# Kernel tuning notes

Measured on AMD Instinct MI355X. Metric: run time of the kernel, lower is better.

## Reference

```python
import jax, jax.numpy as jnp
import numpy as np

B, S, D = 4, 2048, 1024
E, TOPK = 8, 2
SCALE = 0.02


def setup_inputs() -> dict:
    key = jax.random.key(0)
    ks = jax.random.split(key, 7)
    return {
        "x": jax.random.normal(ks[0], (B, S, D), dtype=jnp.float32),
        "router_w": jax.random.normal(ks[1], (D, E), dtype=jnp.float32) * SCALE,
        "router_b": jnp.zeros((E,), dtype=jnp.float32),
        "up_w": jax.random.normal(ks[2], (E, D, 8 * D), dtype=jnp.float32) * SCALE,
        "up_b": jnp.zeros((E, 8 * D), dtype=jnp.float32),
        "down_w": jax.random.normal(ks[3], (E, 4 * D, D), dtype=jnp.float32) * SCALE,
        "down_b": jnp.zeros((E, D), dtype=jnp.float32),
    }


def reference(x, router_w, router_b, up_w, up_b, down_w, down_b):
    b, s, d = x.shape
    flat_x = x.reshape(-1, d)                      # [T, d], T = b*s
    # --- routing ---
    logits = flat_x @ router_w + router_b          # [T, E]
    topk_logits, topk_idx = jax.lax.top_k(logits, TOPK)   # [T, K]
    topk_probs = jax.nn.softmax(topk_logits, axis=-1)     # softmax over the top-k only
    # per-token per-expert combine weight: w[t,e] = sum_k p[t,k] * 1[idx[t,k]==e]
    combine = jnp.sum(
        jax.nn.one_hot(topk_idx, E, dtype=flat_x.dtype) * topk_probs[..., None],
        axis=1,
    )                                              # [T, E]
    # --- experts (dense per-expert compute, masked combine; faithful math) ---
    out = jnp.zeros_like(flat_x)
    for e in range(E):
        h = flat_x @ up_w[e] + up_b[e]             # [T, 8d]
        a, g = jnp.split(h, 2, axis=-1)            # GLU halves, each [T, 4d]
        y = (a * jax.nn.gelu(g, approximate=False)) @ down_w[e] + down_b[e]  # [T, d]
        out = out + combine[:, e:e + 1] * y
    return out.reshape(b, s, d)
```

## Files before the change

### kernel.cpp

```cpp
#include <hip/hip_runtime.h>
#include <hip/hip_bf16.h>

typedef unsigned short u16;
typedef __attribute__((ext_vector_type(8))) short short8;
typedef __attribute__((ext_vector_type(8))) __bf16 bfrag;
typedef __attribute__((ext_vector_type(4))) float cfrag;

#define T_TOK   8192
#define D_MODEL 1024
#define E_EXP   8
#define DFF     4096
#define NPAIR   16384
#define MAXTILE 136

__device__ __forceinline__ u16 f2bf(float f) {
    __hip_bfloat16 h = __float2bfloat16(f);
    return __builtin_bit_cast(u16, h);
}
__device__ __forceinline__ void gld_lds16(const u16* g, u16* l) {
    __builtin_amdgcn_global_load_lds(
        (const __attribute__((address_space(1))) void*)g,
        (__attribute__((address_space(3))) void*)l, 16, 0, 0);
}
__device__ __forceinline__ cfrag mfma16(bfrag a, bfrag b, cfrag c) {
    return __builtin_amdgcn_mfma_f32_16x16x32_bf16(a, b, c, 0, 0, 0);
}

__global__ __launch_bounds__(256) void k_zero(int* cnt) {
    if (threadIdx.x < 64) cnt[threadIdx.x] = 0;
}

__global__ __launch_bounds__(256) void k_route(
    const float* __restrict__ x, const float* __restrict__ rw, const float* __restrict__ rb,
    int* __restrict__ tope, float* __restrict__ wpair, int* __restrict__ cnt)
{
    __shared__ float rws[D_MODEL * E_EXP];
    int tid = threadIdx.x;
    for (int i = tid; i < D_MODEL * E_EXP; i += 256) rws[i] = rw[i];
    __syncthreads();
    int wid = tid >> 6, lane = tid & 63;
    int t = blockIdx.x * 4 + wid;
    const float4* xp = (const float4*)(x + (size_t)t * D_MODEL + lane * 16);
    float xv[16];
#pragma unroll
    for (int j = 0; j < 4; j++) {
        float4 v = xp[j];
        xv[4 * j] = v.x; xv[4 * j + 1] = v.y; xv[4 * j + 2] = v.z; xv[4 * j + 3] = v.w;
    }
    float acc[E_EXP];
#pragma unroll
    for (int e = 0; e < E_EXP; e++) acc[e] = 0.f;
#pragma unroll
    for (int i = 0; i < 16; i++) {
        float xf = xv[i];
        const float* r = &rws[(lane * 16 + i) * E_EXP];
#pragma unroll
        for (int e = 0; e < E_EXP; e++) acc[e] += xf * r[e];
    }
#pragma unroll
    for (int e = 0; e < E_EXP; e++) {
        float v = acc[e];
#pragma unroll
        for (int s = 32; s > 0; s >>= 1) v += __shfl_xor(v, s, 64);
        acc[e] = v;
    }
    if (lane == 0) {
        float lg[E_EXP];
#pragma unroll
        for (int e = 0; e < E_EXP; e++) lg[e] = acc[e] + rb[e];
        int e0 = 0;
        for (int e = 1; e < E_EXP; e++) if (lg[e] > lg[e0]) e0 = e;
        int e1 = -1;
        for (int e = 0; e < E_EXP; e++) {
            if (e == e0) continue;
            if (e1 < 0 || lg[e] > lg[e1]) e1 = e;
        }
        float p0 = 1.f / (1.f + expf(lg[e1] - lg[e0]));
        tope[2 * t] = e0;  tope[2 * t + 1] = e1;
        wpair[2 * t] = p0; wpair[2 * t + 1] = 1.f - p0;
        atomicAdd(&cnt[e0], 1); atomicAdd(&cnt[e1], 1);
    }
}

__global__ void k_scan(const int* __restrict__ cnt, int* __restrict__ cursor,
                       int4* __restrict__ table, int* __restrict__ ntiles)
{
    if (threadIdx.x == 0 && blockIdx.x == 0) {
        int off[E_EXP + 1]; off[0] = 0;
        for (int e = 0; e < E_EXP; e++) off[e + 1] = off[e] + cnt[e];
        for (int e = 0; e < E_EXP; e++) cursor[e] = off[e];
        int nt = 0;
        for (int e = 0; e < E_EXP; e++)
            for (int r = off[e]; r < off[e + 1]; r += 128)
                table[nt++] = make_int4(e, r, off[e + 1], 0);
        *ntiles = nt;
    }
}

__global__ __launch_bounds__(256) void k_permute(
    const int* __restrict__ tope, const float* __restrict__ wpair,
    int* __restrict__ cursor, int* __restrict__ perm,
    int* __restrict__ inv, float* __restrict__ wperm)
{
    int i = blockIdx.x * 256 + threadIdx.x;
    int e = tope[i];
    int p = atomicAdd(&cursor[e], 1);
    perm[p] = i; inv[i] = p; wperm[p] = wpair[i];
}

__global__ __launch_bounds__(256) void k_cvt_x(
    const float* __restrict__ x, u16* __restrict__ xb)
{
    int i = blockIdx.x * 256 + threadIdx.x;
    const float4* xp = (const float4*)(x + (size_t)i * 8);
    float4 v0 = xp[0], v1 = xp[1];
    short8 o;
    o[0] = (short)f2bf(v0.x); o[1] = (short)f2bf(v0.y);
    o[2] = (short)f2bf(v0.z); o[3] = (short)f2bf(v0.w);
    o[4] = (short)f2bf(v1.x); o[5] = (short)f2bf(v1.y);
    o[6] = (short)f2bf(v1.z); o[7] = (short)f2bf(v1.w);
    *(short8*)(xb + (size_t)i * 8) = o;
}

__global__ __launch_bounds__(256) void k_transpose(
    const float* __restrict__ W, u16* __restrict__ WT, int K, int N)
{
    __shared__ u16 tile[64][65];
    int e = blockIdx.z;
    const float* Wp = W + (size_t)e * K * N;
    u16* Tp = WT + (size_t)e * K * N;
    int n0 = blockIdx.x * 64, k0 = blockIdx.y * 64;
    int t = threadIdx.x;
    int rr = t >> 4, cc = (t & 15) * 4;
#pragma unroll
    for (int it = 0; it < 4; ++it) {
        int kr = rr + it * 16;
        float4 v = *(const float4*)(Wp + (size_t)(k0 + kr) * N + n0 + cc);
        tile[kr][cc + 0] = f2bf(v.x); tile[kr][cc + 1] = f2bf(v.y);
        tile[kr][cc + 2] = f2bf(v.z); tile[kr][cc + 3] = f2bf(v.w);
    }
    __syncthreads();
    int nr2 = t >> 3, cc2 = (t & 7) * 8;
#pragma unroll
    for (int it = 0; it < 2; ++it) {
        int nr = nr2 + it * 32;
        short8 v;
#pragma unroll
        for (int i = 0; i < 8; i++) v[i] = (short)tile[cc2 + i][nr];
        *(short8*)(Tp + (size_t)(n0 + nr) * K + k0 + cc2) = v;
    }
}

__global__ __launch_bounds__(256, 2) void k_up_glu(
    const u16* __restrict__ xb, const u16* __restrict__ upT, const float* __restrict__ upb,
    const int* __restrict__ perm, const int4* __restrict__ table,
    const int* __restrict__ ntiles, u16* __restrict__ act)
{
    if ((int)blockIdx.x >= *ntiles) return;
    int4 ti = table[blockIdx.x];
    int e = ti.x, row0 = ti.y, rend = ti.z;
    int n0 = blockIdx.y * 64;
    __shared__ __align__(16) u16 As[128 * 32];
    __shared__ __align__(16) u16 Bs[2][64 * 32];
    int tid = threadIdx.x, lane = tid & 63, wid = tid >> 6;
    int ar = tid >> 2, kc = (tid & 3) * 8;
    int t1 = perm[min(row0 + ar,       rend - 1)] >> 1;
    int t2 = perm[min(row0 + ar + 64,  rend - 1)] >> 1;
    const u16* ga1 = xb + (size_t)t1 * D_MODEL + kc;
    const u16* ga2 = xb + (size_t)t2 * D_MODEL + kc;
    const u16* gb0 = upT + ((size_t)e * 2 * DFF + n0 + ar) * D_MODEL + kc;
    const u16* gb1 = gb0 + (size_t)DFF * D_MODEL;
    u16* lA0 = As + wid * 16 * 32;
    u16* lA1 = As + (64 + wid * 16) * 32;
    u16* lB0 = Bs[0] + wid * 16 * 32;
    u16* lB1 = Bs[1] + wid * 16 * 32;
    cfrag acc[2][4][2];
#pragma unroll
    for (int h = 0; h < 2; h++)
#pragma unroll
        for (int m = 0; m < 4; m++)
#pragma unroll
            for (int n = 0; n < 2; n++) acc[h][m][n] = (cfrag)0.f;
    int wrow = (wid >> 1) * 64, wcol = (wid & 1) * 32;
    int qoff = (lane >> 4) * 8;
    for (int k0 = 0; k0 < D_MODEL; k0 += 32) {
        __syncthreads();
        gld_lds16(ga1, lA0); gld_lds16(ga2, lA1);
        gld_lds16(gb0, lB0); gld_lds16(gb1, lB1);
        ga1 += 32; ga2 += 32; gb0 += 32; gb1 += 32;
        __syncthreads();
        bfrag af[4];
#pragma unroll
        for (int m = 0; m < 4; m++)
            af[m] = __builtin_bit_cast(bfrag, *(const short8*)&As[(wrow + m * 16 + (lane & 15)) * 32 + qoff]);
#pragma unroll
        for (int h = 0; h < 2; h++) {
#pragma unroll
            for (int n = 0; n < 2; n++) {
                bfrag bv = __builtin_bit_cast(bfrag, *(const short8*)&Bs[h][(wcol + n * 16 + (lane & 15)) * 32 + qoff]);
#pragma unroll
                for (int m = 0; m < 4; m++) acc[h][m][n] = mfma16(af[m], bv, acc[h][m][n]);
            }
        }
    }
    const float* ub = upb + (size_t)e * 2 * DFF;
#pragma unroll
    for (int m = 0; m < 4; m++) {
        int rbase = row0 + wrow + m * 16 + ((lane >> 4) << 2);
#pragma unroll
        for (int n = 0; n < 2; n++) {
            int j = n0 + wcol + n * 16 + (lane & 15);
            float ba = ub[j];
            float bg = ub[j + DFF];
#pragma unroll
            for (int r = 0; r < 4; r++) {
                int p = rbase + r;
                if (p < rend) {
                    float a = acc[0][m][n][r] + ba;
                    float g = acc[1][m][n][r] + bg;
                    float gl = 0.5f * g * (1.f + erff(g * 0.70710678118f));
                    act[(size_t)p * DFF + j] = f2bf(a * gl);
                }
            }
        }
    }
}

__global__ __launch_bounds__(256, 2) void k_down(
    const u16* __restrict__ act, const u16* __restrict__ dT, const float* __restrict__ db,
    const float* __restrict__ wperm, const int4* __restrict__ table,
    const int* __restrict__ ntiles, float* __restrict__ ys)
{
    if ((int)blockIdx.x >= *ntiles) return;
    int4 ti = table[blockIdx.x];
    int e = ti.x, row0 = ti.y, rend = ti.z;
    int n0 = blockIdx.y * 128;
    __shared__ __align__(16) u16 As[128 * 32];
    __shared__ __align__(16) u16 Bs[128 * 32];
    int tid = threadIdx.x, lane = tid & 63, wid = tid >> 6;
    int ar = tid >> 2, kc = (tid & 3) * 8;
    int p1 = min(row0 + ar,      rend - 1);
    int p2 = min(row0 + ar + 64, rend - 1);
    const u16* ga1 = act + (size_t)p1 * DFF + kc;
    const u16* ga2 = act + (size_t)p2 * DFF + kc;
    const u16* gb1 = dT + ((size_t)e * D_MODEL + n0 + ar) * DFF + kc;
    const u16* gb2 = gb1 + (size_t)64 * DFF;
    u16* lA0 = As + wid * 16 * 32;
    u16* lA1 = As + (64 + wid * 16) * 32;
    u16* lB0 = Bs + wid * 16 * 32;
    u16* lB1 = Bs + (64 + wid * 16) * 32;
    cfrag acc[4][4];
#pragma unroll
    for (int m = 0; m < 4; m++)
#pragma unroll
        for (int n = 0; n < 4; n++) acc[m][n] = (cfrag)0.f;
    int wrow = (wid >> 1) * 64, wcol = (wid & 1) * 64;
    int qoff = (lane >> 4) * 8;
    for (int k0 = 0; k0 < DFF; k0 += 32) {
        __syncthreads();
        gld_lds16(ga1, lA0); gld_lds16(ga2, lA1);
        gld_lds16(gb1, lB0); gld_lds16(gb2, lB1);
        ga1 += 32; ga2 += 32; gb1 += 32; gb2 += 32;
        __syncthreads();
        bfrag af[4], bv[4];
#pragma unroll
        for (int m = 0; m < 4; m++)
            af[m] = __builtin_bit_cast(bfrag, *(const short8*)&As[(wrow + m * 16 + (lane & 15)) * 32 + qoff]);
#pragma unroll
        for (int n = 0; n < 4; n++)
            bv[n] = __builtin_bit_cast(bfrag, *(const short8*)&Bs[(wcol + n * 16 + (lane & 15)) * 32 + qoff]);
#pragma unroll
        for (int m = 0; m < 4; m++)
#pragma unroll
            for (int n = 0; n < 4; n++) acc[m][n] = mfma16(af[m], bv[n], acc[m][n]);
    }
    const float* dbp = db + (size_t)e * D_MODEL;
#pragma unroll
    for (int m = 0; m < 4; m++) {
        int rbase = row0 + wrow + m * 16 + ((lane >> 4) << 2);
#pragma unroll
        for (int n = 0; n < 4; n++) {
            int col = n0 + wcol + n * 16 + (lane & 15);
            float bias = dbp[col];
#pragma unroll
            for (int r = 0; r < 4; r++) {
                int p = rbase + r;
                if (p < rend)
                    ys[(size_t)p * D_MODEL + col] = (acc[m][n][r] + bias) * wperm[p];
            }
        }
    }
}

__global__ __launch_bounds__(256) void k_combine(
    const float* __restrict__ ys, const int* __restrict__ inv, float* __restrict__ out)
{
    int i = blockIdx.x * 256 + threadIdx.x;
    int t = i >> 8;
    int c = (i & 255) << 2;
    int r0 = inv[2 * t], r1 = inv[2 * t + 1];
    float4 a = *(const float4*)&ys[(size_t)r0 * D_MODEL + c];
    float4 b = *(const float4*)&ys[(size_t)r1 * D_MODEL + c];
    float4 o = make_float4(a.x + b.x, a.y + b.y, a.z + b.z, a.w + b.w);
    *(float4*)&out[(size_t)t * D_MODEL + c] = o;
}

extern "C" void kernel_launch(void* const* d_in, const int* in_sizes, int n_in,
                              void* d_out, int out_size, void* d_ws, size_t ws_size,
                              hipStream_t stream)
{
    const float* x   = (const float*)d_in[0];
    const float* rw  = (const float*)d_in[1];
    const float* rb  = (const float*)d_in[2];
    const float* upw = (const float*)d_in[3];
    const float* upb = (const float*)d_in[4];
    const float* dw  = (const float*)d_in[5];
    const float* db  = (const float*)d_in[6];
    float* out = (float*)d_out;

    char* ws = (char*)d_ws;
    size_t o = 0;
    auto alloc = [&](size_t bytes) -> char* {
        char* p = ws + o; o += (bytes + 255) & ~(size_t)255; return p;
    };
    u16*  upT = (u16*)alloc((size_t)E_EXP * 2 * DFF * D_MODEL * 2);
    u16*  dT  = (u16*)alloc((size_t)E_EXP * D_MODEL * DFF * 2);
    u16*  xb  = (u16*)alloc((size_t)T_TOK * D_MODEL * 2);
    u16*  act = (u16*)alloc((size_t)NPAIR * DFF * 2);
    float* ysb = (float*)upT;
    int*   tope  = (int*)alloc(NPAIR * 4);
    float* wpair = (float*)alloc(NPAIR * 4);
    int*   perm  = (int*)alloc(NPAIR * 4);
    int*   inv   = (int*)alloc(NPAIR * 4);
    float* wperm = (float*)alloc(NPAIR * 4);
    int*   cnt    = (int*)alloc(64 * 4);
    int*   cursor = (int*)alloc(64 * 4);
    int4*  table  = (int4*)alloc(160 * 16);
    int*   ntiles = (int*)alloc(256);
    (void)in_sizes; (void)n_in; (void)out_size; (void)ws_size;

    k_zero<<<1, 256, 0, stream>>>(cnt);
    k_route<<<T_TOK / 4, 256, 0, stream>>>(x, rw, rb, tope, wpair, cnt);
    k_scan<<<1, 64, 0, stream>>>(cnt, cursor, table, ntiles);
    k_permute<<<NPAIR / 256, 256, 0, stream>>>(tope, wpair, cursor, perm, inv, wperm);
    k_cvt_x<<<(T_TOK * D_MODEL / 8) / 256, 256, 0, stream>>>(x, xb);
    k_transpose<<<dim3(8192 / 64, 1024 / 64, E_EXP), 256, 0, stream>>>(upw, upT, 1024, 8192);
    k_transpose<<<dim3(1024 / 64, 4096 / 64, E_EXP), 256, 0, stream>>>(dw, dT, 4096, 1024);
    k_up_glu<<<dim3(MAXTILE, DFF / 64), 256, 0, stream>>>(xb, upT, upb, perm, table, ntiles, act);
    k_down<<<dim3(MAXTILE, D_MODEL / 128), 256, 0, stream>>>(act, dT, db, wperm, table, ntiles, ysb);
    k_combine<<<(T_TOK * D_MODEL / 4) / 256, 256, 0, stream>>>(ysb, inv, out);
}
```

Baseline: 1.481 ms.

## Fuse x bf16 conversion into router and widen GEMM N-tiles

```diff
diff --git a/kernel.cpp b/kernel.cpp
--- a/kernel.cpp
+++ b/kernel.cpp
@@ -32,7 +32,8 @@
 
 __global__ __launch_bounds__(256) void k_route(
     const float* __restrict__ x, const float* __restrict__ rw, const float* __restrict__ rb,
-    int* __restrict__ tope, float* __restrict__ wpair, int* __restrict__ cnt)
+    int* __restrict__ tope, float* __restrict__ wpair, int* __restrict__ cnt,
+    u16* __restrict__ xb)
 {
     __shared__ float rws[D_MODEL * E_EXP];
     int tid = threadIdx.x;
@@ -47,6 +48,13 @@
         float4 v = xp[j];
         xv[4 * j] = v.x; xv[4 * j + 1] = v.y; xv[4 * j + 2] = v.z; xv[4 * j + 3] = v.w;
     }
+    short8 o0, o1;
+#pragma unroll
+    for (int j = 0; j < 8; j++) { o0[j] = (short)f2bf(xv[j]); o1[j] = (short)f2bf(xv[8 + j]); }
+    u16* xbp = xb + (size_t)t * D_MODEL + lane * 16;
+    *(short8*)xbp = o0;
+    *(short8*)(xbp + 8) = o1;
+
     float acc[E_EXP];
 #pragma unroll
     for (int e = 0; e < E_EXP; e++) acc[e] = 0.f;
@@ -108,20 +116,6 @@
     perm[p] = i; inv[i] = p; wperm[p] = wpair[i];
 }
 
-__global__ __launch_bounds__(256) void k_cvt_x(
-    const float* __restrict__ x, u16* __restrict__ xb)
-{
-    int i = blockIdx.x * 256 + threadIdx.x;
-    const float4* xp = (const float4*)(x + (size_t)i * 8);
-    float4 v0 = xp[0], v1 = xp[1];
-    short8 o;
-    o[0] = (short)f2bf(v0.x); o[1] = (short)f2bf(v0.y);
-    o[2] = (short)f2bf(v0.z); o[3] = (short)f2bf(v0.w);
-    o[4] = (short)f2bf(v1.x); o[5] = (short)f2bf(v1.y);
-    o[6] = (short)f2bf(v1.z); o[7] = (short)f2bf(v1.w);
-    *(short8*)(xb + (size_t)i * 8) = o;
-}
-
 __global__ __launch_bounds__(256) void k_transpose(
     const float* __restrict__ W, u16* __restrict__ WT, int K, int N)
 {
@@ -159,35 +153,41 @@
     if ((int)blockIdx.x >= *ntiles) return;
     int4 ti = table[blockIdx.x];
     int e = ti.x, row0 = ti.y, rend = ti.z;
-    int n0 = blockIdx.y * 64;
+    int n0 = blockIdx.y * 128;
     __shared__ __align__(16) u16 As[128 * 32];
-    __shared__ __align__(16) u16 Bs[2][64 * 32];
+    __shared__ __align__(16) u16 Bs[2][128 * 32];
     int tid = threadIdx.x, lane = tid & 63, wid = tid >> 6;
     int ar = tid >> 2, kc = (tid & 3) * 8;
     int t1 = perm[min(row0 + ar,       rend - 1)] >> 1;
     int t2 = perm[min(row0 + ar + 64,  rend - 1)] >> 1;
     const u16* ga1 = xb + (size_t)t1 * D_MODEL + kc;
     const u16* ga2 = xb + (size_t)t2 * D_MODEL + kc;
-    const u16* gb0 = upT + ((size_t)e * 2 * DFF + n0 + ar) * D_MODEL + kc;
-    const u16* gb1 = gb0 + (size_t)DFF * D_MODEL;
-    u16* lA0 = As + wid * 16 * 32;
-    u16* lA1 = As + (64 + wid * 16) * 32;
-    u16* lB0 = Bs[0] + wid * 16 * 32;
-    u16* lB1 = Bs[1] + wid * 16 * 32;
-    cfrag acc[2][4][2];
+    const u16* gb0a = upT + ((size_t)e * 2 * DFF + n0 + ar) * D_MODEL + kc;
+    const u16* gb0b = gb0a + (size_t)64 * D_MODEL;
+    const u16* gb1a = gb0a + (size_t)DFF * D_MODEL;
+    const u16* gb1b = gb1a + (size_t)64 * D_MODEL;
+    u16* lA0  = As + wid * 16 * 32;
+    u16* lA1  = As + (64 + wid * 16) * 32;
+    u16* lB0a = Bs[0] + wid * 16 * 32;
+    u16* lB0b = Bs[0] + (64 + wid * 16) * 32;
+    u16* lB1a = Bs[1] + wid * 16 * 32;
+    u16* lB1b = Bs[1] + (64 + wid * 16) * 32;
+    cfrag acc[2][4][4];
 #pragma unroll
     for (int h = 0; h < 2; h++)
 #pragma unroll
         for (int m = 0; m < 4; m++)
 #pragma unroll
-            for (int n = 0; n < 2; n++) acc[h][m][n] = (cfrag)0.f;
-    int wrow = (wid >> 1) * 64, wcol = (wid & 1) * 32;
+            for (int n = 0; n < 4; n++) acc[h][m][n] = (cfrag)0.f;
+    int wrow = (wid >> 1) * 64, wcol = (wid & 1) * 64;
     int qoff = (lane >> 4) * 8;
     for (int k0 = 0; k0 < D_MODEL; k0 += 32) {
         __syncthreads();
-        gld_lds16(ga1, lA0); gld_lds16(ga2, lA1);
-        gld_lds16(gb0, lB0); gld_lds16(gb1, lB1);
-        ga1 += 32; ga2 += 32; gb0 += 32; gb1 += 32;
+        gld_lds16(ga1, lA0);  gld_lds16(ga2, lA1);
+        gld_lds16(gb0a, lB0a); gld_lds16(gb0b, lB0b);
+        gld_lds16(gb1a, lB1a); gld_lds16(gb1b, lB1b);
+        ga1 += 32; ga2 += 32;
+        gb0a += 32; gb0b += 32; gb1a += 32; gb1b += 32;
         __syncthreads();
         bfrag af[4];
 #pragma unroll
@@ -196,7 +196,7 @@
 #pragma unroll
         for (int h = 0; h < 2; h++) {
 #pragma unroll
-            for (int n = 0; n < 2; n++) {
+            for (int n = 0; n < 4; n++) {
                 bfrag bv = __builtin_bit_cast(bfrag, *(const short8*)&Bs[h][(wcol + n * 16 + (lane & 15)) * 32 + qoff]);
 #pragma unroll
                 for (int m = 0; m < 4; m++) acc[h][m][n] = mfma16(af[m], bv, acc[h][m][n]);
@@ -208,7 +208,7 @@
     for (int m = 0; m < 4; m++) {
         int rbase = row0 + wrow + m * 16 + ((lane >> 4) << 2);
 #pragma unroll
-        for (int n = 0; n < 2; n++) {
+        for (int n = 0; n < 4; n++) {
             int j = n0 + wcol + n * 16 + (lane & 15);
             float ba = ub[j];
             float bg = ub[j + DFF];
@@ -234,52 +234,57 @@
     if ((int)blockIdx.x >= *ntiles) return;
     int4 ti = table[blockIdx.x];
     int e = ti.x, row0 = ti.y, rend = ti.z;
-    int n0 = blockIdx.y * 128;
+    int n0 = blockIdx.y * 256;
     __shared__ __align__(16) u16 As[128 * 32];
-    __shared__ __align__(16) u16 Bs[128 * 32];
+    __shared__ __align__(16) u16 Bs[256 * 32];
     int tid = threadIdx.x, lane = tid & 63, wid = tid >> 6;
     int ar = tid >> 2, kc = (tid & 3) * 8;
     int p1 = min(row0 + ar,      rend - 1);
     int p2 = min(row0 + ar + 64, rend - 1);
     const u16* ga1 = act + (size_t)p1 * DFF + kc;
     const u16* ga2 = act + (size_t)p2 * DFF + kc;
-    const u16* gb1 = dT + ((size_t)e * D_MODEL + n0 + ar) * DFF + kc;
-    const u16* gb2 = gb1 + (size_t)64 * DFF;
+    const u16* gb0 = dT + ((size_t)e * D_MODEL + n0 + ar) * DFF + kc;
+    const u16* gb1 = gb0 + (size_t)64 * DFF;
+    const u16* gb2 = gb0 + (size_t)128 * DFF;
+    const u16* gb3 = gb0 + (size_t)192 * DFF;
     u16* lA0 = As + wid * 16 * 32;
     u16* lA1 = As + (64 + wid * 16) * 32;
-    u16* lB0 = Bs + wid * 16 * 32;
+    u16* lB0 = Bs + (wid * 16) * 32;
     u16* lB1 = Bs + (64 + wid * 16) * 32;
-    cfrag acc[4][4];
+    u16* lB2 = Bs + (128 + wid * 16) * 32;
+    u16* lB3 = Bs + (192 + wid * 16) * 32;
+    cfrag acc[4][8];
 #pragma unroll
     for (int m = 0; m < 4; m++)
 #pragma unroll
-        for (int n = 0; n < 4; n++) acc[m][n] = (cfrag)0.f;
-    int wrow = (wid >> 1) * 64, wcol = (wid & 1) * 64;
+        for (int n = 0; n < 8; n++) acc[m][n] = (cfrag)0.f;
+    int wrow = (wid >> 1) * 64, wcol = (wid & 1) * 128;
     int qoff = (lane >> 4) * 8;
     for (int k0 = 0; k0 < DFF; k0 += 32) {
         __syncthreads();
         gld_lds16(ga1, lA0); gld_lds16(ga2, lA1);
-        gld_lds16(gb1, lB0); gld_lds16(gb2, lB1);
-        ga1 += 32; ga2 += 32; gb1 += 32; gb2 += 32;
+        gld_lds16(gb0, lB0); gld_lds16(gb1, lB1);
+        gld_lds16(gb2, lB2); gld_lds16(gb3, lB3);
+        ga1 += 32; ga2 += 32;
+        gb0 += 32; gb1 += 32; gb2 += 32; gb3 += 32;
         __syncthreads();
-        bfrag af[4], bv[4];
+        bfrag af[4];
 #pragma unroll
         for (int m = 0; m < 4; m++)
             af[m] = __builtin_bit_cast(bfrag, *(const short8*)&As[(wrow + m * 16 + (lane & 15)) * 32 + qoff]);
 #pragma unroll
-        for (int n = 0; n < 4; n++)
-            bv[n] = __builtin_bit_cast(bfrag, *(const short8*)&Bs[(wcol + n * 16 + (lane & 15)) * 32 + qoff]);
-#pragma unroll
-        for (int m = 0; m < 4; m++)
-#pragma unroll
-            for (int n = 0; n < 4; n++) acc[m][n] = mfma16(af[m], bv[n], acc[m][n]);
+        for (int n = 0; n < 8; n++) {
+            bfrag bv = __builtin_bit_cast(bfrag, *(const short8*)&Bs[(wcol + n * 16 + (lane & 15)) * 32 + qoff]);
+#pragma unroll
+            for (int m = 0; m < 4; m++) acc[m][n] = mfma16(af[m], bv, acc[m][n]);
+        }
     }
     const float* dbp = db + (size_t)e * D_MODEL;
 #pragma unroll
     for (int m = 0; m < 4; m++) {
         int rbase = row0 + wrow + m * 16 + ((lane >> 4) << 2);
 #pragma unroll
-        for (int n = 0; n < 4; n++) {
+        for (int n = 0; n < 8; n++) {
             int col = n0 + wcol + n * 16 + (lane & 15);
             float bias = dbp[col];
 #pragma unroll
@@ -340,13 +345,12 @@
     (void)in_sizes; (void)n_in; (void)out_size; (void)ws_size;
 
     k_zero<<<1, 256, 0, stream>>>(cnt);
-    k_route<<<T_TOK / 4, 256, 0, stream>>>(x, rw, rb, tope, wpair, cnt);
+    k_route<<<T_TOK / 4, 256, 0, stream>>>(x, rw, rb, tope, wpair, cnt, xb);
     k_scan<<<1, 64, 0, stream>>>(cnt, cursor, table, ntiles);
     k_permute<<<NPAIR / 256, 256, 0, stream>>>(tope, wpair, cursor, perm, inv, wperm);
-    k_cvt_x<<<(T_TOK * D_MODEL / 8) / 256, 256, 0, stream>>>(x, xb);
     k_transpose<<<dim3(8192 / 64, 1024 / 64, E_EXP), 256, 0, stream>>>(upw, upT, 1024, 8192);
     k_transpose<<<dim3(1024 / 64, 4096 / 64, E_EXP), 256, 0, stream>>>(dw, dT, 4096, 1024);
-    k_up_glu<<<dim3(MAXTILE, DFF / 64), 256, 0, stream>>>(xb, upT, upb, perm, table, ntiles, act);
-    k_down<<<dim3(MAXTILE, D_MODEL / 128), 256, 0, stream>>>(act, dT, db, wperm, table, ntiles, ysb);
+    k_up_glu<<<dim3(MAXTILE, DFF / 128), 256, 0, stream>>>(xb, upT, upb, perm, table, ntiles, act);
+    k_down<<<dim3(MAXTILE, D_MODEL / 256), 256, 0, stream>>>(act, dT, db, wperm, table, ntiles, ysb);
     k_combine<<<(T_TOK * D_MODEL / 4) / 256, 256, 0, stream>>>(ysb, inv, out);
 }
```

Measured after the change: 1.529 ms. 1.03x slower.
